# Performance work log

Hardware: AMD Instinct MI355X
Metric: run time of the kernel (lower is better)

## Reference

```python
import jax, jax.numpy as jnp
import numpy as np

B, T, L = 256, 1024, 128  # batch, seq_len, num_labels


def setup_inputs() -> dict:
    key = jax.random.key(0)
    k1, k2, k3, k4, k5 = jax.random.split(key, 5)
    h = jax.random.normal(k1, (B, T, L), dtype=jnp.float32)
    labels = jax.random.randint(k2, (B, T), 0, L)
    mask = jnp.ones((B, T), dtype=jnp.float32)
    u = lambda k, s: jax.random.uniform(k, s, jnp.float32, -0.1, 0.1)
    trans_matrix = u(k3, (L, L))
    start_trans = u(k4, (L,))
    end_trans = u(k5, (L,))
    return {"h": h, "labels": labels, "mask": mask,
            "trans_matrix": trans_matrix, "start_trans": start_trans,
            "end_trans": end_trans}


def reference(h, labels, mask, trans_matrix, start_trans, end_trans):
    # ---- numerator: score of the gold path ----
    h_y = jnp.take_along_axis(h, labels[..., None], axis=2)[..., 0]      # (B,T)
    trans_y = trans_matrix[labels[:, :-1], labels[:, 1:]]                # (B,T-1)
    num = start_trans[labels[:, 0]]
    num = num + jnp.sum(h_y[:, :-1] * mask[:, :-1] + trans_y * mask[:, 1:], axis=1)
    last_idx = mask.astype(jnp.int32).sum(axis=1) - 1                    # (B,)
    last_labels = jnp.take_along_axis(labels, last_idx[:, None], axis=1)[:, 0]
    # original torch code gathers from h[:, -1] (last timestep), keep faithful
    num = num + jnp.take_along_axis(h[:, -1], last_labels[:, None], axis=1)[:, 0] * mask[:, -1]
    num = num + end_trans[last_labels]

    # ---- denominator: log partition via scan over time ----
    def step(score, inp):
        h_t, m_t = inp  # (B,L), (B,)
        s = jax.nn.logsumexp(score[:, :, None] + h_t[:, None, :] + trans_matrix[None], axis=1)
        m = m_t[:, None]
        return s * m + score * (1.0 - m), None

    score0 = start_trans[None, :] + h[:, 0]                              # (B,L)
    hs = jnp.swapaxes(h, 0, 1)[1:]                                       # (T-1,B,L)
    ms = mask.T[1:]                                                      # (T-1,B)
    scoreT, _ = jax.lax.scan(step, score0, (hs, ms))
    den = jax.nn.logsumexp(scoreT + end_trans[None, :], axis=1)          # (B,)

    return num - den
```

## Files before the change

kernel.cpp:

```cpp
#include <hip/hip_runtime.h>
#include <math.h>

#define Bb 256
#define Tt 1024
#define Ll 128

typedef float v2f __attribute__((ext_vector_type(2)));

__global__ __launch_bounds__(256) void crf_expT_kernel(
    const float* __restrict__ trans, float* __restrict__ expT)
{
    int idx = blockIdx.x * 256 + threadIdx.x;
    if (idx < Ll * Ll) {
        int jj = idx >> 7;
        int ii = idx & (Ll - 1);
        expT[idx] = __expf(trans[ii * Ll + jj]);
    }
}

__global__ __launch_bounds__(256) void crf_num_kernel(
    const float* __restrict__ h, const int* __restrict__ labels,
    const float* __restrict__ mask, const float* __restrict__ trans,
    const float* __restrict__ start_trans, const float* __restrict__ end_trans,
    float* __restrict__ num_out)
{
    const int b = blockIdx.x;
    const int tid = threadIdx.x;
    const int* lab = labels + b * Tt;
    const float* mk = mask + b * Tt;
    const float* hb = h + (size_t)b * Tt * Ll;

    float acc = 0.f;
    float msum = 0.f;
    for (int t = tid; t < Tt; t += 256) {
        int lt = lab[t];
        float mt = mk[t];
        msum += mt;
        if (t < Tt - 1) {
            int lt1 = lab[t + 1];
            acc += hb[t * Ll + lt] * mt + trans[lt * Ll + lt1] * mk[t + 1];
        }
    }
    for (int off = 32; off; off >>= 1) {
        acc  += __shfl_down(acc, off, 64);
        msum += __shfl_down(msum, off, 64);
    }
    __shared__ float racc[4], rmsum[4];
    const int wave = tid >> 6;
    if ((tid & 63) == 0) { racc[wave] = acc; rmsum[wave] = msum; }
    __syncthreads();
    if (tid == 0) {
        float a = racc[0] + racc[1] + racc[2] + racc[3];
        float m = rmsum[0] + rmsum[1] + rmsum[2] + rmsum[3];
        int last_idx = (int)(m + 0.5f) - 1;
        if (last_idx < 0) last_idx = 0;
        if (last_idx > Tt - 1) last_idx = Tt - 1;
        int last_lab = lab[last_idx];
        float num = a + start_trans[lab[0]];
        num += hb[(Tt - 1) * Ll + last_lab] * mk[Tt - 1];
        num += end_trans[last_lab];
        num_out[b] = num;
    }
}

__global__ __launch_bounds__(256)
__attribute__((amdgpu_waves_per_eu(1, 1)))
void crf_den_kernel(
    const float* __restrict__ h, const float* __restrict__ mask,
    const float* __restrict__ expT, const float* __restrict__ start_trans,
    const float* __restrict__ end_trans, const float* __restrict__ num_in,
    float* __restrict__ out)
{
    __shared__ float p_lds[2][160];
    __shared__ float mk_lds[Tt];
    __shared__ float redm[4], reds[4];

    const int b = blockIdx.x;
    const int tid = threadIdx.x;
    const int wave = tid >> 6;
    const int lane = tid & 63;
    const int jgrp = lane >> 3;
    const int isl  = lane & 7;
    const int jbase = (wave << 5) + (jgrp << 2);
    const int wcol  = jbase + (isl & 3);
    const bool writer = (isl < 4);
    const int waddr = wcol + ((wcol >> 4) << 2);

    const float* hb = h + (size_t)b * Tt * Ll;
    const float* mk = mask + b * Tt;

    ((float4*)mk_lds)[tid] = ((const float4*)mk)[tid];

    const v2f* EAp = (const v2f*)(expT + (jbase + 0) * Ll + (isl << 4));
    const v2f* EBp = (const v2f*)(expT + (jbase + 1) * Ll + (isl << 4));
    const v2f* ECp = (const v2f*)(expT + (jbase + 2) * Ll + (isl << 4));
    const v2f* EDp = (const v2f*)(expT + (jbase + 3) * Ll + (isl << 4));
    v2f EA0=EAp[0],EA1=EAp[1],EA2=EAp[2],EA3=EAp[3],EA4=EAp[4],EA5=EAp[5],EA6=EAp[6],EA7=EAp[7];
    v2f EB0=EBp[0],EB1=EBp[1],EB2=EBp[2],EB3=EBp[3],EB4=EBp[4],EB5=EBp[5],EB6=EBp[6],EB7=EBp[7];
    v2f EC0=ECp[0],EC1=ECp[1],EC2=ECp[2],EC3=ECp[3],EC4=ECp[4],EC5=ECp[5],EC6=ECp[6],EC7=ECp[7];
    v2f ED0=EDp[0],ED1=EDp[1],ED2=EDp[2],ED3=EDp[3],ED4=EDp[4],ED5=EDp[5],ED6=EDp[6],ED7=EDp[7];

    float S = start_trans[0] + hb[0] + 16.0f;
    float score0 = start_trans[wcol] + hb[wcol];
    float pw = __expf(score0 - S);
    if (writer) p_lds[0][waddr] = pw;

    float h1 = hb[1 * Ll + wcol], m1 = mk[1];
    float h2 = hb[2 * Ll + wcol], m2 = mk[2];
    float h3 = hb[3 * Ll + wcol], m3 = mk[3];
    float h0 = hb[4 * Ll + wcol], m0 = mk[4];
    __syncthreads();

    float ex1 = __expf(h1) * m1, om1 = 1.f - m1;
    float ex0, om0, ex2, om2, ex3, om3;

#define DPPA(x, ctrl) __int_as_float(__builtin_amdgcn_update_dpp( \
        0, __float_as_int(x), ctrl, 0xF, 0xF, true))

#define PKFMA(A, Q, E) asm("v_pk_fma_f32 %0, %1, %2, %0" : "+v"(A) : "v"(Q), "v"(E));

#define BODY(RBUF, UPD, EXc, OMc, HN, MN, EXn, OMn, HR, MR, TR) {      \
    const float4* pp = (const float4*)(&p_lds[RBUF][isl * 20]);        \
    float4 Q0 = pp[0], Q1 = pp[1], Q2 = pp[2], Q3 = pp[3];             \
    float pz = 0.f;                                                    \
    if (UPD) pz = p_lds[RBUF][0];                                      \
    HR = hb[(TR) * Ll + wcol];                                         \
    MR = mk_lds[(TR)];                                                 \
    v2f q00 = {Q0.x,Q0.y}, q01 = {Q0.z,Q0.w};                          \
    v2f q10 = {Q1.x,Q1.y}, q11 = {Q1.z,Q1.w};                          \
    v2f q20 = {Q2.x,Q2.y}, q21 = {Q2.z,Q2.w};                          \
    v2f q30 = {Q3.x,Q3.y}, q31 = {Q3.z,Q3.w};                          \
    v2f A0 = {0.f,0.f}, A1 = {0.f,0.f}, A2 = {0.f,0.f}, A3 = {0.f,0.f};\
    PKFMA(A0, q00, EA0) PKFMA(A0, q01, EA1) PKFMA(A0, q10, EA2)        \
    PKFMA(A0, q11, EA3) PKFMA(A0, q20, EA4) PKFMA(A0, q21, EA5)        \
    PKFMA(A0, q30, EA6) PKFMA(A0, q31, EA7)                            \
    PKFMA(A1, q00, EB0) PKFMA(A1, q01, EB1) PKFMA(A1, q10, EB2)        \
    PKFMA(A1, q11, EB3) PKFMA(A1, q20, EB4) PKFMA(A1, q21, EB5)        \
    PKFMA(A1, q30, EB6) PKFMA(A1, q31, EB7)                            \
    PKFMA(A2, q00, EC0) PKFMA(A2, q01, EC1) PKFMA(A2, q10, EC2)        \
    PKFMA(A2, q11, EC3) PKFMA(A2, q20, EC4) PKFMA(A2, q21, EC5)        \
    PKFMA(A2, q30, EC6) PKFMA(A2, q31, EC7)                            \
    PKFMA(A3, q00, ED0) PKFMA(A3, q01, ED1) PKFMA(A3, q10, ED2)        \
    PKFMA(A3, q11, ED3) PKFMA(A3, q20, ED4) PKFMA(A3, q21, ED5)        \
    PKFMA(A3, q30, ED6) PKFMA(A3, q31, ED7)                            \
    float a0 = A0.x + A0.y, a1 = A1.x + A1.y;                          \
    float a2 = A2.x + A2.y, a3 = A3.x + A3.y;                          \
    a0 += DPPA(a0,0xB1); a0 += DPPA(a0,0x4E); a0 += DPPA(a0,0x141);    \
    a1 += DPPA(a1,0xB1); a1 += DPPA(a1,0x4E); a1 += DPPA(a1,0x141);    \
    a2 += DPPA(a2,0xB1); a2 += DPPA(a2,0x4E); a2 += DPPA(a2,0x141);    \
    a3 += DPPA(a3,0xB1); a3 += DPPA(a3,0x4E); a3 += DPPA(a3,0x141);    \
    float s01 = (isl & 1) ? a1 : a0;                                   \
    float s23 = (isl & 1) ? a3 : a2;                                   \
    float acc = (isl & 2) ? s23 : s01;                                 \
    float c1 = EXc, c0 = pw * OMc;                                     \
    if (UPD) { float ed = __fdividef(1.12535175e-7f, pz);              \
               c1 *= ed; c0 *= ed; S += __logf(pz) + 16.0f; }          \
    float pn = fmaf(acc, c1, c0);                                      \
    if (writer) p_lds[(RBUF) ^ 1][waddr] = pn;                         \
    EXn = __expf(HN) * MN; OMn = 1.f - MN;                             \
    pw = pn;                                                           \
    __builtin_amdgcn_sched_barrier(0);                                 \
    asm volatile("s_waitcnt lgkmcnt(0)");                              \
    __builtin_amdgcn_s_barrier();                                      \
    __builtin_amdgcn_sched_barrier(0);                                 \
}

    BODY(0, 0, ex1, om1, h2, m2, ex2, om2, h1, m1, 5)
    BODY(1, 0, ex2, om2, h3, m3, ex3, om3, h2, m2, 6)
    BODY(0, 0, ex3, om3, h0, m0, ex0, om0, h3, m3, 7)

    for (int k = 1; k < 255; ++k) {
        int t4 = k << 2;
        BODY(1, 1, ex0, om0, h1, m1, ex1, om1, h0, m0, t4 + 4)
        BODY(0, 0, ex1, om1, h2, m2, ex2, om2, h1, m1, t4 + 5)
        BODY(1, 0, ex2, om2, h3, m3, ex3, om3, h2, m2, t4 + 6)
        BODY(0, 0, ex3, om3, h0, m0, ex0, om0, h3, m3, t4 + 7)
    }
    BODY(1, 1, ex0, om0, h1, m1, ex1, om1, h0, m0, Tt - 1)
    BODY(0, 0, ex1, om1, h2, m2, ex2, om2, h1, m1, Tt - 1)
    BODY(1, 0, ex2, om2, h3, m3, ex3, om3, h2, m2, Tt - 1)
    BODY(0, 0, ex3, om3, h0, m0, ex0, om0, h3, m3, Tt - 1)
#undef BODY
#undef PKFMA
#undef DPPA

    float v = __logf(pw) + S + end_trans[wcol];
    float mval = writer ? v : -1e30f;
    #pragma unroll
    for (int off = 32; off; off >>= 1) mval = fmaxf(mval, __shfl_xor(mval, off, 64));
    if (lane == 0) redm[wave] = mval;
    __syncthreads();
    float M = fmaxf(fmaxf(redm[0], redm[1]), fmaxf(redm[2], redm[3]));
    float e = writer ? __expf(v - M) : 0.f;
    #pragma unroll
    for (int off = 32; off; off >>= 1) e += __shfl_xor(e, off, 64);
    if (lane == 0) reds[wave] = e;
    __syncthreads();
    if (tid == 0) {
        float den = M + __logf(reds[0] + reds[1] + reds[2] + reds[3]);
        out[b] = num_in[b] - den;
    }
}

extern "C" void kernel_launch(void* const* d_in, const int* in_sizes, int n_in,
                              void* d_out, int out_size, void* d_ws, size_t ws_size,
                              hipStream_t stream) {
    const float* h           = (const float*)d_in[0];
    const int*   labels      = (const int*)d_in[1];
    const float* mask        = (const float*)d_in[2];
    const float* trans       = (const float*)d_in[3];
    const float* start_trans = (const float*)d_in[4];
    const float* end_trans   = (const float*)d_in[5];
    float* out    = (float*)d_out;
    float* num_ws = (float*)d_ws;
    float* expT   = (float*)d_ws + 256;

    crf_expT_kernel<<<(Ll * Ll + 255) / 256, 256, 0, stream>>>(trans, expT);
    crf_num_kernel<<<Bb, 256, 0, stream>>>(h, labels, mask, trans, start_trans, end_trans, num_ws);
    crf_den_kernel<<<Bb, 256, 0, stream>>>(h, mask, expT, start_trans, end_trans, num_ws, out);
}
```

Before: 256.1 us.

## Split den recurrence across 512 threads with 16-lane partial dot products

Doubles the block size of the denominator kernel to 512 threads. Each 16-lane group now computes 4 output labels with 8-element partial dot products instead of 16, and the DPP reduction gains one extra step. The LDS layout of the probability vector changes padding to suit the new access pattern. The hand-written packed-FMA asm is replaced with vector expressions the compiler can schedule. The goal is to shorten the per-timestep critical path of the sequential scan. In exchange, each step now needs a barrier across 8 waves and a longer reduction chain.

Measured after the change: 308.2 us. +20.3%, slower.

```diff
diff --git a/kernel.cpp b/kernel.cpp
--- a/kernel.cpp
+++ b/kernel.cpp
@@ -63,42 +63,42 @@
     }
 }
 
-__global__ __launch_bounds__(256)
-__attribute__((amdgpu_waves_per_eu(1, 1)))
+__global__ __launch_bounds__(512)
+__attribute__((amdgpu_waves_per_eu(2, 2)))
 void crf_den_kernel(
     const float* __restrict__ h, const float* __restrict__ mask,
     const float* __restrict__ expT, const float* __restrict__ start_trans,
     const float* __restrict__ end_trans, const float* __restrict__ num_in,
     float* __restrict__ out)
 {
-    __shared__ float p_lds[2][160];
+    __shared__ float p_lds[2][192];
     __shared__ float mk_lds[Tt];
-    __shared__ float redm[4], reds[4];
+    __shared__ float redm[8], reds[8];
 
     const int b = blockIdx.x;
     const int tid = threadIdx.x;
     const int wave = tid >> 6;
     const int lane = tid & 63;
-    const int jgrp = lane >> 3;
-    const int isl  = lane & 7;
-    const int jbase = (wave << 5) + (jgrp << 2);
+    const int cg   = lane >> 4;
+    const int isl  = lane & 15;
+    const int jbase = (wave << 4) + (cg << 2);
     const int wcol  = jbase + (isl & 3);
     const bool writer = (isl < 4);
-    const int waddr = wcol + ((wcol >> 4) << 2);
+    const int waddr = (wcol >> 3) * 12 + (wcol & 7);
 
     const float* hb = h + (size_t)b * Tt * Ll;
     const float* mk = mask + b * Tt;
 
-    ((float4*)mk_lds)[tid] = ((const float4*)mk)[tid];
-
-    const v2f* EAp = (const v2f*)(expT + (jbase + 0) * Ll + (isl << 4));
-    const v2f* EBp = (const v2f*)(expT + (jbase + 1) * Ll + (isl << 4));
-    const v2f* ECp = (const v2f*)(expT + (jbase + 2) * Ll + (isl << 4));
-    const v2f* EDp = (const v2f*)(expT + (jbase + 3) * Ll + (isl << 4));
-    v2f EA0=EAp[0],EA1=EAp[1],EA2=EAp[2],EA3=EAp[3],EA4=EAp[4],EA5=EAp[5],EA6=EAp[6],EA7=EAp[7];
-    v2f EB0=EBp[0],EB1=EBp[1],EB2=EBp[2],EB3=EBp[3],EB4=EBp[4],EB5=EBp[5],EB6=EBp[6],EB7=EBp[7];
-    v2f EC0=ECp[0],EC1=ECp[1],EC2=ECp[2],EC3=ECp[3],EC4=ECp[4],EC5=ECp[5],EC6=ECp[6],EC7=ECp[7];
-    v2f ED0=EDp[0],ED1=EDp[1],ED2=EDp[2],ED3=EDp[3],ED4=EDp[4],ED5=EDp[5],ED6=EDp[6],ED7=EDp[7];
+    if (tid < 256) ((float4*)mk_lds)[tid] = ((const float4*)mk)[tid];
+
+    const v2f* EAp = (const v2f*)(expT + (jbase + 0) * Ll + (isl << 3));
+    const v2f* EBp = (const v2f*)(expT + (jbase + 1) * Ll + (isl << 3));
+    const v2f* ECp = (const v2f*)(expT + (jbase + 2) * Ll + (isl << 3));
+    const v2f* EDp = (const v2f*)(expT + (jbase + 3) * Ll + (isl << 3));
+    v2f EA0=EAp[0],EA1=EAp[1],EA2=EAp[2],EA3=EAp[3];
+    v2f EB0=EBp[0],EB1=EBp[1],EB2=EBp[2],EB3=EBp[3];
+    v2f EC0=ECp[0],EC1=ECp[1],EC2=ECp[2],EC3=ECp[3];
+    v2f ED0=EDp[0],ED1=EDp[1],ED2=EDp[2],ED3=EDp[3];
 
     float S = start_trans[0] + hb[0] + 16.0f;
     float score0 = start_trans[wcol] + hb[wcol];
@@ -115,40 +115,31 @@
     float ex0, om0, ex2, om2, ex3, om3;
 
 #define DPPA(x, ctrl) __int_as_float(__builtin_amdgcn_update_dpp( \
-        0, __float_as_int(x), ctrl, 0xF, 0xF, true))
-
-#define PKFMA(A, Q, E) asm("v_pk_fma_f32 %0, %1, %2, %0" : "+v"(A) : "v"(Q), "v"(E));
+        __float_as_int(x), __float_as_int(x), ctrl, 0xF, 0xF, true))
 
 #define BODY(RBUF, UPD, EXc, OMc, HN, MN, EXn, OMn, HR, MR, TR) {      \
-    const float4* pp = (const float4*)(&p_lds[RBUF][isl * 20]);        \
-    float4 Q0 = pp[0], Q1 = pp[1], Q2 = pp[2], Q3 = pp[3];             \
+    const float4* pp = (const float4*)(&p_lds[RBUF][isl * 12]);        \
+    float4 Q0 = pp[0], Q1 = pp[1];                                     \
     float pz = 0.f;                                                    \
     if (UPD) pz = p_lds[RBUF][0];                                      \
     HR = hb[(TR) * Ll + wcol];                                         \
     MR = mk_lds[(TR)];                                                 \
-    v2f q00 = {Q0.x,Q0.y}, q01 = {Q0.z,Q0.w};                          \
-    v2f q10 = {Q1.x,Q1.y}, q11 = {Q1.z,Q1.w};                          \
-    v2f q20 = {Q2.x,Q2.y}, q21 = {Q2.z,Q2.w};                          \
-    v2f q30 = {Q3.x,Q3.y}, q31 = {Q3.z,Q3.w};                          \
-    v2f A0 = {0.f,0.f}, A1 = {0.f,0.f}, A2 = {0.f,0.f}, A3 = {0.f,0.f};\
-    PKFMA(A0, q00, EA0) PKFMA(A0, q01, EA1) PKFMA(A0, q10, EA2)        \
-    PKFMA(A0, q11, EA3) PKFMA(A0, q20, EA4) PKFMA(A0, q21, EA5)        \
-    PKFMA(A0, q30, EA6) PKFMA(A0, q31, EA7)                            \
-    PKFMA(A1, q00, EB0) PKFMA(A1, q01, EB1) PKFMA(A1, q10, EB2)        \
-    PKFMA(A1, q11, EB3) PKFMA(A1, q20, EB4) PKFMA(A1, q21, EB5)        \
-    PKFMA(A1, q30, EB6) PKFMA(A1, q31, EB7)                            \
-    PKFMA(A2, q00, EC0) PKFMA(A2, q01, EC1) PKFMA(A2, q10, EC2)        \
-    PKFMA(A2, q11, EC3) PKFMA(A2, q20, EC4) PKFMA(A2, q21, EC5)        \
-    PKFMA(A2, q30, EC6) PKFMA(A2, q31, EC7)                            \
-    PKFMA(A3, q00, ED0) PKFMA(A3, q01, ED1) PKFMA(A3, q10, ED2)        \
-    PKFMA(A3, q11, ED3) PKFMA(A3, q20, ED4) PKFMA(A3, q21, ED5)        \
-    PKFMA(A3, q30, ED6) PKFMA(A3, q31, ED7)                            \
+    v2f q0 = {Q0.x,Q0.y}, q1 = {Q0.z,Q0.w};                            \
+    v2f q2 = {Q1.x,Q1.y}, q3 = {Q1.z,Q1.w};                            \
+    v2f A0 = q0*EA0; A0 = q1*EA1 + A0; A0 = q2*EA2 + A0; A0 = q3*EA3 + A0; \
+    v2f A1 = q0*EB0; A1 = q1*EB1 + A1; A1 = q2*EB2 + A1; A1 = q3*EB3 + A1; \
+    v2f A2 = q0*EC0; A2 = q1*EC1 + A2; A2 = q2*EC2 + A2; A2 = q3*EC3 + A2; \
+    v2f A3 = q0*ED0; A3 = q1*ED1 + A3; A3 = q2*ED2 + A3; A3 = q3*ED3 + A3; \
     float a0 = A0.x + A0.y, a1 = A1.x + A1.y;                          \
     float a2 = A2.x + A2.y, a3 = A3.x + A3.y;                          \
-    a0 += DPPA(a0,0xB1); a0 += DPPA(a0,0x4E); a0 += DPPA(a0,0x141);    \
-    a1 += DPPA(a1,0xB1); a1 += DPPA(a1,0x4E); a1 += DPPA(a1,0x141);    \
-    a2 += DPPA(a2,0xB1); a2 += DPPA(a2,0x4E); a2 += DPPA(a2,0x141);    \
-    a3 += DPPA(a3,0xB1); a3 += DPPA(a3,0x4E); a3 += DPPA(a3,0x141);    \
+    a0 += DPPA(a0,0xB1); a0 += DPPA(a0,0x4E);                          \
+    a0 += DPPA(a0,0x141); a0 += DPPA(a0,0x140);                        \
+    a1 += DPPA(a1,0xB1); a1 += DPPA(a1,0x4E);                          \
+    a1 += DPPA(a1,0x141); a1 += DPPA(a1,0x140);                        \
+    a2 += DPPA(a2,0xB1); a2 += DPPA(a2,0x4E);                          \
+    a2 += DPPA(a2,0x141); a2 += DPPA(a2,0x140);                        \
+    a3 += DPPA(a3,0xB1); a3 += DPPA(a3,0x4E);                          \
+    a3 += DPPA(a3,0x141); a3 += DPPA(a3,0x140);                        \
     float s01 = (isl & 1) ? a1 : a0;                                   \
     float s23 = (isl & 1) ? a3 : a2;                                   \
     float acc = (isl & 2) ? s23 : s01;                                 \
@@ -181,7 +172,6 @@
     BODY(1, 0, ex2, om2, h3, m3, ex3, om3, h2, m2, Tt - 1)
     BODY(0, 0, ex3, om3, h0, m0, ex0, om0, h3, m3, Tt - 1)
 #undef BODY
-#undef PKFMA
 #undef DPPA
 
     float v = __logf(pw) + S + end_trans[wcol];
@@ -190,14 +180,16 @@
     for (int off = 32; off; off >>= 1) mval = fmaxf(mval, __shfl_xor(mval, off, 64));
     if (lane == 0) redm[wave] = mval;
     __syncthreads();
-    float M = fmaxf(fmaxf(redm[0], redm[1]), fmaxf(redm[2], redm[3]));
+    float M = fmaxf(fmaxf(fmaxf(redm[0], redm[1]), fmaxf(redm[2], redm[3])),
+                    fmaxf(fmaxf(redm[4], redm[5]), fmaxf(redm[6], redm[7])));
     float e = writer ? __expf(v - M) : 0.f;
     #pragma unroll
     for (int off = 32; off; off >>= 1) e += __shfl_xor(e, off, 64);
     if (lane == 0) reds[wave] = e;
     __syncthreads();
     if (tid == 0) {
-        float den = M + __logf(reds[0] + reds[1] + reds[2] + reds[3]);
+        float den = M + __logf(reds[0] + reds[1] + reds[2] + reds[3] +
+                               reds[4] + reds[5] + reds[6] + reds[7]);
         out[b] = num_in[b] - den;
     }
 }
@@ -217,5 +209,5 @@
 
     crf_expT_kernel<<<(Ll * Ll + 255) / 256, 256, 0, stream>>>(trans, expT);
     crf_num_kernel<<<Bb, 256, 0, stream>>>(h, labels, mask, trans, start_trans, end_trans, num_ws);
-    crf_den_kernel<<<Bb, 256, 0, stream>>>(h, mask, expT, start_trans, end_trans, num_ws, out);
-}
+    crf_den_kernel<<<Bb, 512, 0, stream>>>(h, mask, expT, start_trans, end_trans, num_ws, out);
+}
```
